# Performance work log

Hardware: AMD Instinct MI355X
Metric: run time of the kernel (lower is better)

The kernel has to match this reference:

```python
import jax, jax.numpy as jnp
import numpy as np

H = 1024


def _trilinear(q, k, w1, w2, w3):
    # q: [B, Lq, H], k: [B, Lk, H], w*: [H]
    ql = q @ w1                                  # [B, Lq]
    kl = k @ w2                                  # [B, Lk]
    dot = jnp.einsum('bqd,bkd->bqk', q, k * w3)  # [B, Lq, Lk]
    return ql[:, :, None] + kl[:, None, :] + dot


def _attention(q, k, v, qm, km, w1, w2, w3):
    # qm: [B, Lq] bool, km: [B, Lk] bool
    logit = _trilinear(q, k, w1, w2, w3)
    mask = qm[:, :, None] & km[:, None, :]
    logit = jnp.where(mask, logit, -jnp.inf)
    aw = jnp.where(mask, jax.nn.softmax(logit, axis=-1), 0.0)   # row softmax
    attn = aw @ v
    kq = jnp.where(mask, jax.nn.softmax(logit, axis=1), 0.0)    # column softmax
    co_w = aw @ jnp.swapaxes(kq, -1, -2)                        # [B, Lq, Lq]
    co_attn = co_w @ q
    return attn, co_attn


def setup_inputs() -> dict:
    key = jax.random.key(0)
    ks = jax.random.split(key, 20)
    B, S = 32, 1024
    def lin(k, out_d, in_d):
        kw, kb = jax.random.split(k)
        return (jax.random.normal(kw, (out_d, in_d), jnp.float32) * 0.02,
                jnp.zeros((out_d,), jnp.float32))
    comp_w, comp_b = lin(ks[3], H, 7 * H)
    gate_w, gate_b = lin(ks[4], H, 2 * H)
    attn_w, attn_b = lin(ks[5], H, 3 * H)
    self_w, self_b = lin(ks[6], H, 4 * H)
    tri = lambda k: jax.random.normal(k, (H,), jnp.float32) * 0.02
    return {
        'input_ids': jax.random.randint(ks[0], (B, S), 0, 30000, jnp.int32),
        'attention_mask': jnp.ones((B, S), jnp.int32),
        'doc_final_pos': 769,
        'num_label': 4,
        'last_layer': jax.random.normal(ks[1], (B, S, H), jnp.float32),
        'ow1': tri(ks[7]), 'ow2': tri(ks[8]), 'ow3': tri(ks[9]),
        'dw1': tri(ks[10]), 'dw2': tri(ks[11]), 'dw3': tri(ks[12]),
        'sw1': tri(ks[13]), 'sw2': tri(ks[14]), 'sw3': tri(ks[15]),
        'comp_w': comp_w, 'comp_b': comp_b,
        'gate_w': gate_w, 'gate_b': gate_b,
        'attn_w': attn_w, 'attn_b': attn_b,
        'self_w': self_w, 'self_b': self_b,
    }


def reference(input_ids, attention_mask, doc_final_pos, num_label, last_layer,
              ow1, ow2, ow3, dw1, dw2, dw3, sw1, sw2, sw3,
              comp_w, comp_b, gate_w, gate_b, attn_w, attn_b, self_w, self_b):
    bsz = input_ids.shape[0] // num_label
    p = doc_final_pos
    h = last_layer.shape[-1]
    doc_enc = last_layer[:, : p - 1, :]            # [B, Ld, H]
    opt_enc = last_layer[:, p - 1 :, :]            # [B, Lo, H]
    Lo = opt_enc.shape[1]
    doc_mask = attention_mask[:, : p - 1] > 0
    opt_mask4 = (attention_mask[:, p - 1 :] > 0).reshape(bsz, num_label, Lo)
    opt_enc4 = opt_enc.reshape(bsz, num_label, Lo, h)
    # pairwise option comparison
    corr = []
    for i in range(num_label):
        cur, cm = opt_enc4[:, i], opt_mask4[:, i]
        comp = [cur]
        for j in range(num_label):
            if j == i:
                continue
            a, _ = _attention(cur, opt_enc4[:, j], opt_enc4[:, j], cm, opt_mask4[:, j], ow1, ow2, ow3)
            comp.append(cur * a)
            comp.append(cur - a)
        corr.append(jnp.tanh(jnp.concatenate(comp, -1) @ comp_w.T + comp_b))
    opt_corr = jnp.stack(corr, axis=1).reshape(bsz * num_label, Lo, h)
    om = opt_mask4.reshape(bsz * num_label, Lo)
    gate = jax.nn.sigmoid(jnp.concatenate([opt_enc, opt_corr], -1) @ gate_w.T + gate_b)
    option = opt_enc * gate + opt_corr * (1.0 - gate)
    a, co = _attention(option, doc_enc, doc_enc, om, doc_mask, dw1, dw2, dw3)
    fusion = jax.nn.relu(jnp.concatenate([option, a, co], -1) @ attn_w.T + attn_b)
    sa, _ = _attention(fusion, fusion, fusion, om, om, sw1, sw2, sw3)
    fusion = jax.nn.relu(jnp.concatenate([fusion, sa, fusion * sa, fusion - sa], -1) @ self_w.T + self_b)
    fusion = jnp.where(om[:, :, None], fusion, -jnp.inf)
    return fusion.max(axis=1)  # [bsz*num_label, H]
```

## Files before the change

kernel.cpp:

```cpp
#include <hip/hip_runtime.h>

#define HDIM 1024
#define LLBS 1048576L
#define OPTBS 262144L
#define LDSP 72

typedef _Float16 f16;
typedef __attribute__((ext_vector_type(8))) _Float16 f16x8;
typedef __attribute__((ext_vector_type(4))) _Float16 f16x4;
typedef __attribute__((ext_vector_type(4))) float    f32x4;

__global__ __launch_bounds__(256)
void cvt_kernel(const float* __restrict__ src, f16* __restrict__ dst, long n)
{
  long i = ((long)blockIdx.x * 256 + threadIdx.x) * 8;
  const long stride = (long)gridDim.x * 256 * 8;
  for (; i < n; i += stride) {
    const float4 a = *(const float4*)(src + i);
    const float4 b = *(const float4*)(src + i + 4);
    *(f16x8*)(dst + i) = f16x8{(f16)a.x,(f16)a.y,(f16)a.z,(f16)a.w,
                               (f16)b.x,(f16)b.y,(f16)b.z,(f16)b.w};
  }
}

__device__ __forceinline__
void stage_rows(f16* __restrict__ sh, const f16* __restrict__ src, long rs, int t)
{
  const int row = t >> 1, h = (t & 1) << 5;
  const f16x8* p = (const f16x8*)(src + (long)row * rs + h);
  const f16x8 a = p[0], b = p[1], c = p[2], d = p[3];
  f16x8* q = (f16x8*)&sh[row * LDSP + h];
  q[0] = a; q[1] = b; q[2] = c; q[3] = d;
}

__device__ __forceinline__ f16x8 sc8(f16x8 v, const float* s)
{
  const float4 s0 = *(const float4*)s, s1 = *(const float4*)(s + 4);
  f16x8 r;
  r[0]=(f16)((float)v[0]*s0.x); r[1]=(f16)((float)v[1]*s0.y);
  r[2]=(f16)((float)v[2]*s0.z); r[3]=(f16)((float)v[3]*s0.w);
  r[4]=(f16)((float)v[4]*s1.x); r[5]=(f16)((float)v[5]*s1.y);
  r[6]=(f16)((float)v[6]*s1.z); r[7]=(f16)((float)v[7]*s1.w);
  return r;
}

__device__ __forceinline__
void stage_rows_scale(f16* __restrict__ sh, const f16* __restrict__ src, long rs,
                      const float* __restrict__ sc, int t)
{
  const int row = t >> 1, h = (t & 1) << 5;
  const f16x8* p = (const f16x8*)(src + (long)row * rs + h);
  f16x8* q = (f16x8*)&sh[row * LDSP + h];
  #pragma unroll
  for (int e = 0; e < 4; ++e) q[e] = sc8(p[e], sc + h + e * 8);
}

__device__ __forceinline__
void stage_vt(f16* __restrict__ sh, const f16* __restrict__ src, long rs, int t)
{
  const int jc = (t & 31) << 2, kg = (t >> 5) << 3;
  const f16* p = src + (long)kg * rs + jc;
  f16x4 r[8];
  #pragma unroll
  for (int e = 0; e < 8; ++e) r[e] = *(const f16x4*)(p + (long)e * rs);
  #pragma unroll
  for (int c = 0; c < 4; ++c) {
    *(f16x8*)&sh[(jc + c) * LDSP + kg] =
      f16x8{r[0][c], r[1][c], r[2][c], r[3][c], r[4][c], r[5][c], r[6][c], r[7][c]};
  }
}

__device__ __forceinline__
void mfma_step(const f16* __restrict__ Ash, const f16* __restrict__ Bsh, int t, f32x4 acc[4][4])
{
  const int lane = t & 63, wid = t >> 6;
  const int wm = (wid >> 1) << 6, wn = (wid & 1) << 6;
  const int r = lane & 15;
  #pragma unroll
  for (int kh = 0; kh < 2; ++kh) {
    const int kg = (kh << 5) + ((lane >> 4) << 3);
    f16x8 af[4], bf[4];
    #pragma unroll
    for (int m = 0; m < 4; ++m) af[m] = *(const f16x8*)&Ash[(wm + m * 16 + r) * LDSP + kg];
    #pragma unroll
    for (int n = 0; n < 4; ++n) bf[n] = *(const f16x8*)&Bsh[(wn + n * 16 + r) * LDSP + kg];
    #pragma unroll
    for (int m = 0; m < 4; ++m)
      #pragma unroll
      for (int n = 0; n < 4; ++n)
        acc[m][n] = __builtin_amdgcn_mfma_f32_16x16x32_f16(af[m], bf[n], acc[m][n], 0, 0, 0);
  }
}

template<int SCALE>
__device__ __forceinline__
void mm_at_core(f16* Ash, f16* Bsh, const f16* Ab, long Ars,
                const f16* Bb, long Brs, int K, const float* scale, int t, f32x4 acc[4][4])
{
  for (int k0 = 0; k0 < K; k0 += 64) {
    __syncthreads();
    stage_rows(Ash, Ab + k0, Ars, t);
    if (SCALE) stage_rows_scale(Bsh, Bb + k0, Brs, scale + k0, t);
    else       stage_rows(Bsh, Bb + k0, Brs, t);
    __syncthreads();
    mfma_step(Ash, Bsh, t, acc);
  }
}

__device__ __forceinline__
void mm_ab_core(f16* Ash, f16* Bsh, const f16* Ab, long Ars,
                const f16* Bb, long Brs, int K, int t, f32x4 acc[4][4])
{
  for (int k0 = 0; k0 < K; k0 += 64) {
    __syncthreads();
    stage_rows(Ash, Ab + k0, Ars, t);
    stage_vt(Bsh, Bb + (long)k0 * Brs, Brs, t);
    __syncthreads();
    mfma_step(Ash, Bsh, t, acc);
  }
}

template<int SCALE, int RANK1, int HOUT>
__global__ __launch_bounds__(256)
void mm_at_kernel(const f16* __restrict__ A, long Abs, long Ars,
                  const f16* __restrict__ B, long Bbs, long Brs, int K,
                  const float* __restrict__ scale,
                  const float* __restrict__ ql, long qlbs,
                  const float* __restrict__ kl, long klbs,
                  void* __restrict__ C, long Cbs, long Crs)
{
  __shared__ __align__(16) f16 Ash[128 * LDSP];
  __shared__ __align__(16) f16 Bsh[128 * LDSP];
  const int z = blockIdx.z, t = threadIdx.x;
  const int i0 = blockIdx.y << 7, j0 = blockIdx.x << 7;
  f32x4 acc[4][4] = {};
  mm_at_core<SCALE>(Ash, Bsh, A + (long)z * Abs + (long)i0 * Ars, Ars,
                    B + (long)z * Bbs + (long)j0 * Brs, Brs, K, scale, t, acc);
  const int lane = t & 63, wid = t >> 6;
  const int wm = (wid >> 1) << 6, wn = (wid & 1) << 6;
  const int rq = (lane >> 4) << 2, cj = lane & 15;
  #pragma unroll
  for (int m = 0; m < 4; ++m)
    #pragma unroll
    for (int q = 0; q < 4; ++q) {
      const int row = i0 + wm + m * 16 + rq + q;
      const float qv = RANK1 ? ql[(long)z * qlbs + row] : 0.f;
      #pragma unroll
      for (int n = 0; n < 4; ++n) {
        const int col = j0 + wn + n * 16 + cj;
        float v = acc[m][n][q] + qv;
        if (RANK1) v += kl[(long)z * klbs + col];
        if (HOUT) ((f16*)C)[(long)z * Cbs + (long)row * Crs + col] = (f16)v;
        else      ((float*)C)[(long)z * Cbs + (long)row * Crs + col] = v;
      }
    }
}

__global__ __launch_bounds__(256)
void mm_ab_kernel(const f16* __restrict__ A, long Abs, long Ars,
                  const f16* __restrict__ B, long Bbs, long Brs, int K,
                  f16* __restrict__ C, long Cbs, long Crs)
{
  __shared__ __align__(16) f16 Ash[128 * LDSP];
  __shared__ __align__(16) f16 Bsh[128 * LDSP];
  const int z = blockIdx.z, t = threadIdx.x;
  const int i0 = blockIdx.y << 7, j0 = blockIdx.x << 7;
  f32x4 acc[4][4] = {};
  mm_ab_core(Ash, Bsh, A + (long)z * Abs + (long)i0 * Ars, Ars,
             B + (long)z * Bbs + j0, Brs, K, t, acc);
  const int lane = t & 63, wid = t >> 6;
  const int wm = (wid >> 1) << 6, wn = (wid & 1) << 6;
  const int rq = (lane >> 4) << 2, cj = lane & 15;
  f16* Cb = C + (long)z * Cbs;
  #pragma unroll
  for (int m = 0; m < 4; ++m)
    #pragma unroll
    for (int q = 0; q < 4; ++q) {
      const int row = i0 + wm + m * 16 + rq + q;
      #pragma unroll
      for (int n = 0; n < 4; ++n) {
        const int col = j0 + wn + n * 16 + cj;
        Cb[(long)row * Crs + col] = (f16)acc[m][n][q];
      }
    }
}

__device__ __forceinline__ void pair_decode(int pair, int& i, int& j) {
  i = pair / 3; const int r = pair - i * 3; j = r + (r >= i ? 1 : 0);
}

__global__ __launch_bounds__(256)
void stA_logits_kernel(const f16* __restrict__ OPT, const float* __restrict__ w3,
                       const float* __restrict__ ql_all, const float* __restrict__ kl_all,
                       float* __restrict__ L)
{
  __shared__ __align__(16) f16 Ash[128 * LDSP];
  __shared__ __align__(16) f16 Bsh[128 * LDSP];
  const int z = blockIdx.z, t = threadIdx.x;
  const int pair = z >> 3, b8 = z & 7;
  int i, j; pair_decode(pair, i, j);
  const int bi = b8 * 4 + i, bj = b8 * 4 + j;
  const int i0 = blockIdx.y << 7, j0 = blockIdx.x << 7;
  f32x4 acc[4][4] = {};
  mm_at_core<1>(Ash, Bsh, OPT + (long)bi * LLBS + (long)i0 * HDIM, HDIM,
                OPT + (long)bj * LLBS + (long)j0 * HDIM, HDIM, HDIM, w3, t, acc);
  const float* qlp = ql_all + bi * 256;
  const float* klp = kl_all + bj * 256;
  float* Cb = L + (long)z * 65536;
  const int lane = t & 63, wid = t >> 6;
  const int wm = (wid >> 1) << 6, wn = (wid & 1) << 6;
  const int rq = (lane >> 4) << 2, cj = lane & 15;
  #pragma unroll
  for (int m = 0; m < 4; ++m)
    #pragma unroll
    for (int q = 0; q < 4; ++q) {
      const int row = i0 + wm + m * 16 + rq + q;
      const float qv = qlp[row];
      #pragma unroll
      for (int n = 0; n < 4; ++n) {
        const int col = j0 + wn + n * 16 + cj;
        Cb[(long)row * 256 + col] = acc[m][n][q] + qv + klp[col];
      }
    }
}

__global__ __launch_bounds__(256)
void stA_attn_kernel(const f16* __restrict__ P, const f16* __restrict__ OPT,
                     f16* __restrict__ aBuf)
{
  __shared__ __align__(16) f16 Ash[128 * LDSP];
  __shared__ __align__(16) f16 Bsh[128 * LDSP];
  const int z = blockIdx.z, t = threadIdx.x;
  const int pair = z >> 3, b8 = z & 7;
  int i, j; pair_decode(pair, i, j);
  const int bj = b8 * 4 + j;
  const int i0 = blockIdx.y << 7, j0 = blockIdx.x << 7;
  f32x4 acc[4][4] = {};
  mm_ab_core(Ash, Bsh, P + (long)z * 65536 + (long)i0 * 256, 256,
             OPT + (long)bj * LLBS + j0, HDIM, 256, t, acc);
  const int lane = t & 63, wid = t >> 6;
  const int wm = (wid >> 1) << 6, wn = (wid & 1) << 6;
  const int rq = (lane >> 4) << 2, cj = lane & 15;
  f16* Cb = aBuf + (long)z * OPTBS;
  #pragma unroll
  for (int m = 0; m < 4; ++m)
    #pragma unroll
    for (int q = 0; q < 4; ++q) {
      const int row = i0 + wm + m * 16 + rq + q;
      #pragma unroll
      for (int n = 0; n < 4; ++n)
        Cb[(long)row * HDIM + j0 + wn + n * 16 + cj] = (f16)acc[m][n][q];
    }
}

__global__ __launch_bounds__(256)
void stA_comp_kernel(const f16* __restrict__ OPT, const f16* __restrict__ aBuf,
                     const f16* __restrict__ W, const float* __restrict__ bias,
                     f16* __restrict__ out)
{
  __shared__ __align__(16) f16 Ash[128 * LDSP];
  __shared__ __align__(16) f16 Wsh[128 * LDSP];
  const int Lb = blockIdx.x, t = threadIdx.x;
  const int c = Lb & 7, w = Lb >> 3;
  const int n0 = (w >> 3) << 7;
  const int g = (c << 3) | (w & 7);
  const int i0 = (g & 1) << 7;
  const int z = g >> 1;
  const int b8 = z >> 2, i = z & 3;
  const f16* cur = OPT + (long)z * LLBS;
  const f16* a0 = aBuf + (long)((i * 3 + 0) * 8 + b8) * OPTBS;
  const f16* a1 = aBuf + (long)((i * 3 + 1) * 8 + b8) * OPTBS;
  const f16* a2 = aBuf + (long)((i * 3 + 2) * 8 + b8) * OPTBS;
  const f16* Wb = W + (long)n0 * 7168;
  f32x4 acc[4][4] = {};
  const int row = t >> 1, h = (t & 1) << 5;
  for (int k0 = 0; k0 < 7168; k0 += 64) {
    const int blk = k0 >> 10, kk = k0 & 1023;
    __syncthreads();
    {
      const long ro = (long)(i0 + row) * HDIM + kk + h;
      const f16x8* pc = (const f16x8*)(cur + ro);
      f16x8 a = pc[0], b = pc[1], cc = pc[2], d = pc[3];
      if (blk) {
        const int m = (blk - 1) >> 1;
        const f16* ap = (m == 0) ? a0 : (m == 1 ? a1 : a2);
        const f16x8* pa = (const f16x8*)(ap + ro);
        const f16x8 e = pa[0], f = pa[1], gg = pa[2], hh = pa[3];
        if (blk & 1) { a *= e; b *= f; cc *= gg; d *= hh; }
        else         { a -= e; b -= f; cc -= gg; d -= hh; }
      }
      f16x8* q = (f16x8*)&Ash[row * LDSP + h];
      q[0] = a; q[1] = b; q[2] = cc; q[3] = d;
    }
    stage_rows(Wsh, Wb + k0, 7168, t);
    __syncthreads();
    mfma_step(Ash, Wsh, t, acc);
  }
  const int lane = t & 63, wid = t >> 6;
  const int wm = (wid >> 1) << 6, wn = (wid & 1) << 6;
  const int rq = (lane >> 4) << 2, cj = lane & 15;
  f16* ob = out + (long)z * OPTBS;
  #pragma unroll
  for (int m = 0; m < 4; ++m)
    #pragma unroll
    for (int q = 0; q < 4; ++q) {
      const int r2 = i0 + wm + m * 16 + rq + q;
      #pragma unroll
      for (int n = 0; n < 4; ++n) {
        const int col = n0 + wn + n * 16 + cj;
        ob[(long)r2 * HDIM + col] = (f16)tanhf(acc[m][n][q] + bias[col]);
      }
    }
}

struct FCSrc { const f16* s0; const f16* s1; long s0bs; long s1bs; int op; int pad; };
struct FCArgs {
  FCSrc src[4];
  int nblk; int act;
  const f16* W; const float* bias;
  f16* out; long outbs;
  const f16* e0; const f16* e1; long e0bs; long e1bs;
};

__global__ __launch_bounds__(256)
void fc_mfma_kernel(FCArgs P)
{
  __shared__ __align__(16) f16 Ash[128 * LDSP];
  __shared__ __align__(16) f16 Wsh[128 * LDSP];
  const int Lb = blockIdx.x, t = threadIdx.x;
  const int c = Lb & 7, w = Lb >> 3;
  const int n0 = (w >> 3) << 7;
  const int g = (c << 3) | (w & 7);
  const int i0 = (g & 1) << 7;
  const int b = g >> 1;
  const int Ktot = P.nblk << 10;
  const f16* Wb = P.W + (long)n0 * Ktot;
  f32x4 acc[4][4] = {};
  const int row = t >> 1, h = (t & 1) << 5;
  for (int k0 = 0; k0 < Ktot; k0 += 64) {
    const FCSrc s = P.src[k0 >> 10];
    const int kk = k0 & 1023;
    __syncthreads();
    {
      const long ro = (long)(i0 + row) * HDIM + kk + h;
      const f16x8* p0 = (const f16x8*)(s.s0 + (long)b * s.s0bs + ro);
      f16x8 a = p0[0], bb = p0[1], cc = p0[2], d = p0[3];
      if (s.op) {
        const f16x8* p1 = (const f16x8*)(s.s1 + (long)b * s.s1bs + ro);
        const f16x8 e = p1[0], f = p1[1], gg = p1[2], hh = p1[3];
        if (s.op == 1) { a *= e; bb *= f; cc *= gg; d *= hh; }
        else           { a -= e; bb -= f; cc -= gg; d -= hh; }
      }
      f16x8* q = (f16x8*)&Ash[row * LDSP + h];
      q[0] = a; q[1] = bb; q[2] = cc; q[3] = d;
    }
    stage_rows(Wsh, Wb + k0, Ktot, t);
    __syncthreads();
    mfma_step(Ash, Wsh, t, acc);
  }
  const int lane = t & 63, wid = t >> 6;
  const int wm = (wid >> 1) << 6, wn = (wid & 1) << 6;
  const int rq = (lane >> 4) << 2, cj = lane & 15;
  #pragma unroll
  for (int m = 0; m < 4; ++m)
    #pragma unroll
    for (int q = 0; q < 4; ++q) {
      const int r2 = i0 + wm + m * 16 + rq + q;
      f16* orow = P.out + (long)b * P.outbs + (long)r2 * HDIM;
      #pragma unroll
      for (int n = 0; n < 4; ++n) {
        const int col = n0 + wn + n * 16 + cj;
        float v = acc[m][n][q] + P.bias[col];
        if (P.act == 0) v = tanhf(v);
        else if (P.act == 1) v = fmaxf(v, 0.f);
        else {
          const float sg = 1.f / (1.f + __expf(-v));
          const float e = (float)P.e0[(long)b * P.e0bs + (long)r2 * HDIM + col];
          const float c2 = (float)P.e1[(long)b * P.e1bs + (long)r2 * HDIM + col];
          v = e * sg + c2 * (1.f - sg);
        }
        orow[col] = (f16)v;
      }
    }
}

__global__ __launch_bounds__(256)
void rowdot_kernel(const f16* __restrict__ base, long bs, int R,
                   const float* __restrict__ w, float* __restrict__ out)
{
  const int row  = blockIdx.x * 4 + (threadIdx.x >> 6);
  const int lane = threadIdx.x & 63;
  const int b = row / R, r = row - b * R;
  const f16* p = base + (long)b * bs + (long)r * HDIM;
  float s = 0.f;
  #pragma unroll 4
  for (int d = lane; d < HDIM; d += 64) s += (float)p[d] * w[d];
  #pragma unroll
  for (int off = 32; off; off >>= 1) s += __shfl_down(s, off, 64);
  if (lane == 0) out[row] = s;
}

template<int CNT>
__global__ __launch_bounds__(256)
void softmax_rows_kernel(const float* __restrict__ L, f16* __restrict__ P)
{
  const int row = blockIdx.x * 4 + (threadIdx.x >> 6);
  const int lane = threadIdx.x & 63;
  const float* p = L + (long)row * (CNT * 64);
  f16* o = P + (long)row * (CNT * 64);
  float v[CNT];
  float m = -3.0e38f;
  #pragma unroll
  for (int u = 0; u < CNT; ++u) { v[u] = p[lane + (u << 6)]; m = fmaxf(m, v[u]); }
  #pragma unroll
  for (int off = 32; off; off >>= 1) m = fmaxf(m, __shfl_xor(m, off, 64));
  float s = 0.f;
  #pragma unroll
  for (int u = 0; u < CNT; ++u) { v[u] = __expf(v[u] - m); s += v[u]; }
  #pragma unroll
  for (int off = 32; off; off >>= 1) s += __shfl_xor(s, off, 64);
  const float inv = 1.f / s;
  #pragma unroll
  for (int u = 0; u < CNT; ++u) o[lane + (u << 6)] = (f16)(v[u] * inv);
}

__global__ __launch_bounds__(256)
void softmax_cols_kernel(const float* __restrict__ L, f16* __restrict__ out, int M, int N)
{
  const int b = blockIdx.y;
  const int j = blockIdx.x * 256 + threadIdx.x;
  const float* p = L + (long)b * M * N + j;
  f16* o = out + (long)b * M * N + j;
  float m = -3.0e38f;
  for (int i = 0; i < M; ++i) m = fmaxf(m, p[(long)i * N]);
  float s = 0.f;
  for (int i = 0; i < M; ++i) { const float e = __expf(p[(long)i * N] - m); o[(long)i * N] = (f16)e; s += e; }
  const float inv = 1.f / s;
  for (int i = 0; i < M; ++i) o[(long)i * N] = (f16)((float)o[(long)i * N] * inv);
}

__global__ __launch_bounds__(256)
void colmax_kernel(const f16* __restrict__ X, float* __restrict__ out)
{
  const int b = blockIdx.y;
  const int d = blockIdx.x * 256 + threadIdx.x;
  const f16* p = X + (long)b * (256 * HDIM) + d;
  float m = -3.0e38f;
  for (int r = 0; r < 256; ++r) m = fmaxf(m, (float)p[r * HDIM]);
  out[b * HDIM + d] = m;
}

extern "C" void kernel_launch(void* const* d_in, const int* in_sizes, int n_in,
                              void* d_out, int out_size, void* d_ws, size_t ws_size,
                              hipStream_t stream)
{
  (void)in_sizes; (void)n_in; (void)out_size; (void)ws_size;
  const float* last   = (const float*)d_in[4];
  const float* ow1    = (const float*)d_in[5];
  const float* ow2    = (const float*)d_in[6];
  const float* ow3    = (const float*)d_in[7];
  const float* dw1    = (const float*)d_in[8];
  const float* dw2    = (const float*)d_in[9];
  const float* dw3    = (const float*)d_in[10];
  const float* sw1    = (const float*)d_in[11];
  const float* sw2    = (const float*)d_in[12];
  const float* sw3    = (const float*)d_in[13];
  const float* comp_w = (const float*)d_in[14];
  const float* comp_b = (const float*)d_in[15];
  const float* gate_w = (const float*)d_in[16];
  const float* gate_b = (const float*)d_in[17];
  const float* attn_w = (const float*)d_in[18];
  const float* attn_b = (const float*)d_in[19];
  const float* self_w = (const float*)d_in[20];
  const float* self_b = (const float*)d_in[21];

  char* base = (char*)d_ws;
  size_t off = 0;
  auto af = [&](long n) { float* p = (float*)(base + off); off = (off + n * 4 + 15) & ~15UL; return p; };
  auto ah = [&](long n) { f16* p = (f16*)(base + off); off = (off + n * 2 + 15) & ~15UL; return p; };

  f16* lastH = ah(33554432L);
  f16* compH = ah(7340032L);
  f16* gateH = ah(2097152L);
  f16* attnH = ah(3145728L);
  f16* selfH = ah(4194304L);
  f16* aBuf  = ah(96L * OPTBS);
  f16* pA    = ah(96L * 65536);
  f16* awC   = ah(32L * 196608);
  f16* kqC   = ah(32L * 196608);
  f16* pE    = ah(32L * 65536);
  f16* co_wH = ah(32L * 65536);
  f16* buf1  = ah(32L * OPTBS);
  f16* buf2  = ah(32L * OPTBS);
  f16* buf3  = ah(32L * OPTBS);
  f16* buf4  = ah(32L * OPTBS);
  float* L   = af(32L * 196608);
  float* ql_all = af(8192); float* kl_all = af(8192);
  float* ql_c   = af(8192); float* kl_c   = af(24576);
  float* ql_e   = af(8192); float* kl_e   = af(8192);

  const f16* OPTH = lastH + 768 * 1024;

  cvt_kernel<<<2048, 256, 0, stream>>>(last,   lastH, 33554432L);
  cvt_kernel<<<512,  256, 0, stream>>>(comp_w, compH, 7340032L);
  cvt_kernel<<<256,  256, 0, stream>>>(gate_w, gateH, 2097152L);
  cvt_kernel<<<256,  256, 0, stream>>>(attn_w, attnH, 3145728L);
  cvt_kernel<<<256,  256, 0, stream>>>(self_w, selfH, 4194304L);

  rowdot_kernel<<<2048, 256, 0, stream>>>(OPTH, LLBS, 256, ow1, ql_all);
  rowdot_kernel<<<2048, 256, 0, stream>>>(OPTH, LLBS, 256, ow2, kl_all);
  stA_logits_kernel<<<dim3(2, 2, 96), 256, 0, stream>>>(OPTH, ow3, ql_all, kl_all, L);
  softmax_rows_kernel<4><<<(96 * 256) / 4, 256, 0, stream>>>(L, pA);
  stA_attn_kernel<<<dim3(8, 2, 96), 256, 0, stream>>>(pA, OPTH, aBuf);
  stA_comp_kernel<<<512, 256, 0, stream>>>(OPTH, aBuf, compH, comp_b, buf1);

  {
    FCArgs P = {};
    P.src[0] = {OPTH, nullptr, LLBS,  0, 0, 0};
    P.src[1] = {buf1, nullptr, OPTBS, 0, 0, 0};
    P.nblk = 2; P.act = 2; P.W = gateH; P.bias = gate_b;
    P.e0 = OPTH; P.e0bs = LLBS; P.e1 = buf1; P.e1bs = OPTBS;
    P.out = buf2; P.outbs = OPTBS;
    fc_mfma_kernel<<<512, 256, 0, stream>>>(P);
  }

  rowdot_kernel<<<2048, 256, 0, stream>>>(buf2, OPTBS, 256, dw1, ql_c);
  rowdot_kernel<<<6144, 256, 0, stream>>>(lastH, LLBS, 768, dw2, kl_c);
  mm_at_kernel<1, 1, 0><<<dim3(6, 2, 32), 256, 0, stream>>>(buf2, OPTBS, HDIM, lastH, LLBS, HDIM, HDIM,
                                                            dw3, ql_c, 256, kl_c, 768, L, 196608, 768);
  softmax_cols_kernel<<<dim3(3, 32), 256, 0, stream>>>(L, kqC, 256, 768);
  softmax_rows_kernel<12><<<8192 / 4, 256, 0, stream>>>(L, awC);
  mm_ab_kernel<<<dim3(8, 2, 32), 256, 0, stream>>>(awC, 196608, 768, lastH, LLBS, HDIM, 768,
                                                   buf1, OPTBS, HDIM);
  mm_at_kernel<0, 0, 1><<<dim3(2, 2, 32), 256, 0, stream>>>(awC, 196608, 768, kqC, 196608, 768, 768,
                                                            nullptr, nullptr, 0, nullptr, 0, co_wH, 65536, 256);
  mm_ab_kernel<<<dim3(8, 2, 32), 256, 0, stream>>>(co_wH, 65536, 256, buf2, OPTBS, HDIM, 256,
                                                   buf3, OPTBS, HDIM);

  {
    FCArgs P = {};
    P.src[0] = {buf2, nullptr, OPTBS, 0, 0, 0};
    P.src[1] = {buf1, nullptr, OPTBS, 0, 0, 0};
    P.src[2] = {buf3, nullptr, OPTBS, 0, 0, 0};
    P.nblk = 3; P.act = 1; P.W = attnH; P.bias = attn_b;
    P.out = buf4; P.outbs = OPTBS;
    fc_mfma_kernel<<<512, 256, 0, stream>>>(P);
  }

  rowdot_kernel<<<2048, 256, 0, stream>>>(buf4, OPTBS, 256, sw1, ql_e);
  rowdot_kernel<<<2048, 256, 0, stream>>>(buf4, OPTBS, 256, sw2, kl_e);
  mm_at_kernel<1, 1, 0><<<dim3(2, 2, 32), 256, 0, stream>>>(buf4, OPTBS, HDIM, buf4, OPTBS, HDIM, HDIM,
                                                            sw3, ql_e, 256, kl_e, 256, L, 65536, 256);
  softmax_rows_kernel<4><<<8192 / 4, 256, 0, stream>>>(L, pE);
  mm_ab_kernel<<<dim3(8, 2, 32), 256, 0, stream>>>(pE, 65536, 256, buf4, OPTBS, HDIM, 256,
                                                   buf2, OPTBS, HDIM);

  {
    FCArgs P = {};
    P.src[0] = {buf4, nullptr, OPTBS, 0, 0, 0};
    P.src[1] = {buf2, nullptr, OPTBS, 0, 0, 0};
    P.src[2] = {buf4, buf2, OPTBS, OPTBS, 1, 0};
    P.src[3] = {buf4, buf2, OPTBS, OPTBS, 2, 0};
    P.nblk = 4; P.act = 1; P.W = selfH; P.bias = self_b;
    P.out = buf3; P.outbs = OPTBS;
    fc_mfma_kernel<<<512, 256, 0, stream>>>(P);
  }

  colmax_kernel<<<dim3(4, 32), 256, 0, stream>>>(buf3, (float*)d_out);
}
```

Measured before the change: 1.348 ms.

## Double-buffer GEMM LDS tiles with async global-to-LDS loads and XOR swizzle

Every MFMA GEMM kernel now uses two LDS buffers per operand. The next K-slice is fetched while the current one feeds the MFMAs, leaving one barrier per iteration instead of two. Plain operand tiles are loaded straight into LDS with global_load_lds, and the padded layout is replaced by an XOR-swizzled 128-byte row layout to avoid bank conflicts. LDS use doubles to 64KB per block, which may reduce occupancy.

```diff
diff --git a/kernel.cpp b/kernel.cpp
--- a/kernel.cpp
+++ b/kernel.cpp
@@ -3,70 +3,82 @@
 #define HDIM 1024
 #define LLBS 1048576L
 #define OPTBS 262144L
-#define LDSP 72
 
 typedef _Float16 f16;
 typedef __attribute__((ext_vector_type(8))) _Float16 f16x8;
 typedef __attribute__((ext_vector_type(4))) _Float16 f16x4;
 typedef __attribute__((ext_vector_type(4))) float    f32x4;
 
-__global__ __launch_bounds__(256)
-void cvt_kernel(const float* __restrict__ src, f16* __restrict__ dst, long n)
-{
-  long i = ((long)blockIdx.x * 256 + threadIdx.x) * 8;
-  const long stride = (long)gridDim.x * 256 * 8;
-  for (; i < n; i += stride) {
-    const float4 a = *(const float4*)(src + i);
-    const float4 b = *(const float4*)(src + i + 4);
-    *(f16x8*)(dst + i) = f16x8{(f16)a.x,(f16)a.y,(f16)a.z,(f16)a.w,
-                               (f16)b.x,(f16)b.y,(f16)b.z,(f16)b.w};
-  }
+__device__ __forceinline__ char* swzp(f16* tile, int row, int colb) {
+  return (char*)tile + (row << 7) + (colb ^ ((row & 7) << 4));
+}
+__device__ __forceinline__ const char* swzp(const f16* tile, int row, int colb) {
+  return (const char*)tile + (row << 7) + (colb ^ ((row & 7) << 4));
+}
+
+__device__ __forceinline__ void gload16(const f16* g, f16* l) {
+  __builtin_amdgcn_global_load_lds((const __attribute__((address_space(1))) void*)g,
+                                   (__attribute__((address_space(3))) void*)l, 16, 0, 0);
 }
 
 __device__ __forceinline__
-void stage_rows(f16* __restrict__ sh, const f16* __restrict__ src, long rs, int t)
-{
-  const int row = t >> 1, h = (t & 1) << 5;
-  const f16x8* p = (const f16x8*)(src + (long)row * rs + h);
-  const f16x8 a = p[0], b = p[1], c = p[2], d = p[3];
-  f16x8* q = (f16x8*)&sh[row * LDSP + h];
-  q[0] = a; q[1] = b; q[2] = c; q[3] = d;
-}
-
-__device__ __forceinline__ f16x8 sc8(f16x8 v, const float* s)
-{
-  const float4 s0 = *(const float4*)s, s1 = *(const float4*)(s + 4);
-  f16x8 r;
-  r[0]=(f16)((float)v[0]*s0.x); r[1]=(f16)((float)v[1]*s0.y);
-  r[2]=(f16)((float)v[2]*s0.z); r[3]=(f16)((float)v[3]*s0.w);
-  r[4]=(f16)((float)v[4]*s1.x); r[5]=(f16)((float)v[5]*s1.y);
-  r[6]=(f16)((float)v[6]*s1.z); r[7]=(f16)((float)v[7]*s1.w);
-  return r;
-}
-
-__device__ __forceinline__
-void stage_rows_scale(f16* __restrict__ sh, const f16* __restrict__ src, long rs,
-                      const float* __restrict__ sc, int t)
-{
-  const int row = t >> 1, h = (t & 1) << 5;
-  const f16x8* p = (const f16x8*)(src + (long)row * rs + h);
-  f16x8* q = (f16x8*)&sh[row * LDSP + h];
-  #pragma unroll
-  for (int e = 0; e < 4; ++e) q[e] = sc8(p[e], sc + h + e * 8);
-}
-
-__device__ __forceinline__
-void stage_vt(f16* __restrict__ sh, const f16* __restrict__ src, long rs, int t)
-{
+void stage_g(f16* __restrict__ tile, const f16* __restrict__ src, long rs, int t)
+{
+  const int l = t & 63, w = t >> 6;
+  const int rsub = l >> 3;
+  const int csub = ((l & 7) ^ rsub) << 3;
+  const f16* gp = src + (long)rsub * rs + csub;
+  #pragma unroll
+  for (int p = 0; p < 4; ++p) {
+    const int i = (w << 2) + p;
+    gload16(gp + (long)(i << 3) * rs, tile + (i << 9));
+  }
+}
+
+struct VT { f16x4 r[8]; };
+__device__ __forceinline__ VT vt_load(const f16* __restrict__ src, long rs, int t) {
   const int jc = (t & 31) << 2, kg = (t >> 5) << 3;
   const f16* p = src + (long)kg * rs + jc;
-  f16x4 r[8];
-  #pragma unroll
-  for (int e = 0; e < 8; ++e) r[e] = *(const f16x4*)(p + (long)e * rs);
-  #pragma unroll
-  for (int c = 0; c < 4; ++c) {
-    *(f16x8*)&sh[(jc + c) * LDSP + kg] =
-      f16x8{r[0][c], r[1][c], r[2][c], r[3][c], r[4][c], r[5][c], r[6][c], r[7][c]};
+  VT v;
+  #pragma unroll
+  for (int e = 0; e < 8; ++e) v.r[e] = *(const f16x4*)(p + (long)e * rs);
+  return v;
+}
+__device__ __forceinline__ void vt_write(f16* __restrict__ tile, const VT& v, int t) {
+  const int jc = (t & 31) << 2, kg = (t >> 5) << 3;
+  #pragma unroll
+  for (int c = 0; c < 4; ++c)
+    *(f16x8*)swzp(tile, jc + c, kg << 1) =
+      f16x8{v.r[0][c], v.r[1][c], v.r[2][c], v.r[3][c],
+            v.r[4][c], v.r[5][c], v.r[6][c], v.r[7][c]};
+}
+
+__device__ __forceinline__ void ld4(f16x8 v[4], const f16* p) {
+  const f16x8* q = (const f16x8*)p;
+  v[0] = q[0]; v[1] = q[1]; v[2] = q[2]; v[3] = q[3];
+}
+__device__ __forceinline__ void a_write(f16* __restrict__ tile, const f16x8 v[4], int t) {
+  const int row = t >> 1, h2 = (t & 1) << 6;
+  #pragma unroll
+  for (int e = 0; e < 4; ++e)
+    *(f16x8*)swzp(tile, row, h2 + (e << 4)) = v[e];
+}
+__device__ __forceinline__
+void sc_load(f16x8 v[4], const f16* __restrict__ src, long rs,
+             const float* __restrict__ sc, int t)
+{
+  const int row = t >> 1, h = (t & 1) << 5;
+  ld4(v, src + (long)row * rs + h);
+  #pragma unroll
+  for (int e = 0; e < 4; ++e) {
+    const float4 s0 = *(const float4*)(sc + h + e * 8);
+    const float4 s1 = *(const float4*)(sc + h + e * 8 + 4);
+    f16x8 x = v[e];
+    x[0]=(f16)((float)x[0]*s0.x); x[1]=(f16)((float)x[1]*s0.y);
+    x[2]=(f16)((float)x[2]*s0.z); x[3]=(f16)((float)x[3]*s0.w);
+    x[4]=(f16)((float)x[4]*s1.x); x[5]=(f16)((float)x[5]*s1.y);
+    x[6]=(f16)((float)x[6]*s1.z); x[7]=(f16)((float)x[7]*s1.w);
+    v[e] = x;
   }
 }
 
@@ -78,12 +90,12 @@
   const int r = lane & 15;
   #pragma unroll
   for (int kh = 0; kh < 2; ++kh) {
-    const int kg = (kh << 5) + ((lane >> 4) << 3);
+    const int kb = ((kh << 5) | ((lane >> 4) << 3)) << 1;
     f16x8 af[4], bf[4];
     #pragma unroll
-    for (int m = 0; m < 4; ++m) af[m] = *(const f16x8*)&Ash[(wm + m * 16 + r) * LDSP + kg];
-    #pragma unroll
-    for (int n = 0; n < 4; ++n) bf[n] = *(const f16x8*)&Bsh[(wn + n * 16 + r) * LDSP + kg];
+    for (int m = 0; m < 4; ++m) af[m] = *(const f16x8*)swzp(Ash, wm + m * 16 + r, kb);
+    #pragma unroll
+    for (int n = 0; n < 4; ++n) bf[n] = *(const f16x8*)swzp(Bsh, wn + n * 16 + r, kb);
     #pragma unroll
     for (int m = 0; m < 4; ++m)
       #pragma unroll
@@ -92,50 +104,60 @@
   }
 }
 
-template<int SCALE>
+template<int BMODE>
 __device__ __forceinline__
-void mm_at_core(f16* Ash, f16* Bsh, const f16* Ab, long Ars,
-                const f16* Bb, long Brs, int K, const float* scale, int t, f32x4 acc[4][4])
-{
-  for (int k0 = 0; k0 < K; k0 += 64) {
+void mm_body(f16* A0, f16* A1, f16* B0, f16* B1,
+             const f16* __restrict__ Ab, long Ars,
+             const f16* __restrict__ Bb, long Brs, int K,
+             const float* __restrict__ scale, int t, f32x4 acc[4][4])
+{
+  stage_g(A0, Ab, Ars, t);
+  if (BMODE == 1) { VT v = vt_load(Bb, Brs, t); vt_write(B0, v, t); }
+  else if (BMODE == 2) { f16x8 v[4]; sc_load(v, Bb, Brs, scale, t); a_write(B0, v, t); }
+  else stage_g(B0, Bb, Brs, t);
+  __syncthreads();
+  f16 *Ac = A0, *An = A1, *Bc = B0, *Bn = B1;
+  for (int k0 = 64; k0 < K; k0 += 64) {
+    stage_g(An, Ab + k0, Ars, t);
+    if (BMODE == 1) {
+      VT v = vt_load(Bb + (long)k0 * Brs, Brs, t);
+      mfma_step(Ac, Bc, t, acc);
+      vt_write(Bn, v, t);
+    } else if (BMODE == 2) {
+      f16x8 v[4]; sc_load(v, Bb + k0, Brs, scale + k0, t);
+      mfma_step(Ac, Bc, t, acc);
+      a_write(Bn, v, t);
+    } else {
+      stage_g(Bn, Bb + k0, Brs, t);
+      mfma_step(Ac, Bc, t, acc);
+    }
     __syncthreads();
-    stage_rows(Ash, Ab + k0, Ars, t);
-    if (SCALE) stage_rows_scale(Bsh, Bb + k0, Brs, scale + k0, t);
-    else       stage_rows(Bsh, Bb + k0, Brs, t);
-    __syncthreads();
-    mfma_step(Ash, Bsh, t, acc);
-  }
-}
-
-__device__ __forceinline__
-void mm_ab_core(f16* Ash, f16* Bsh, const f16* Ab, long Ars,
-                const f16* Bb, long Brs, int K, int t, f32x4 acc[4][4])
-{
-  for (int k0 = 0; k0 < K; k0 += 64) {
-    __syncthreads();
-    stage_rows(Ash, Ab + k0, Ars, t);
-    stage_vt(Bsh, Bb + (long)k0 * Brs, Brs, t);
-    __syncthreads();
-    mfma_step(Ash, Bsh, t, acc);
-  }
-}
-
-template<int SCALE, int RANK1, int HOUT>
-__global__ __launch_bounds__(256)
-void mm_at_kernel(const f16* __restrict__ A, long Abs, long Ars,
-                  const f16* __restrict__ B, long Bbs, long Brs, int K,
-                  const float* __restrict__ scale,
-                  const float* __restrict__ ql, long qlbs,
-                  const float* __restrict__ kl, long klbs,
-                  void* __restrict__ C, long Cbs, long Crs)
-{
-  __shared__ __align__(16) f16 Ash[128 * LDSP];
-  __shared__ __align__(16) f16 Bsh[128 * LDSP];
+    f16* x = Ac; Ac = An; An = x; x = Bc; Bc = Bn; Bn = x;
+  }
+  mfma_step(Ac, Bc, t, acc);
+}
+
+#define DECL_TILES \
+  __shared__ __align__(16) f16 A0[8192]; __shared__ __align__(16) f16 A1[8192]; \
+  __shared__ __align__(16) f16 B0[8192]; __shared__ __align__(16) f16 B1[8192];
+
+template<int BMODE, int RANK1, int HOUT>
+__global__ __launch_bounds__(256)
+void mm_kernel(const f16* __restrict__ A, long Abs, long Ars,
+               const f16* __restrict__ B, long Bbs, long Brs, int K,
+               const float* __restrict__ scale,
+               const float* __restrict__ ql, long qlbs,
+               const float* __restrict__ kl, long klbs,
+               void* __restrict__ C, long Cbs, long Crs)
+{
+  DECL_TILES
   const int z = blockIdx.z, t = threadIdx.x;
   const int i0 = blockIdx.y << 7, j0 = blockIdx.x << 7;
+  const f16* Ab = A + (long)z * Abs + (long)i0 * Ars;
+  const f16* Bb = (BMODE == 1) ? (B + (long)z * Bbs + j0)
+                               : (B + (long)z * Bbs + (long)j0 * Brs);
   f32x4 acc[4][4] = {};
-  mm_at_core<SCALE>(Ash, Bsh, A + (long)z * Abs + (long)i0 * Ars, Ars,
-                    B + (long)z * Bbs + (long)j0 * Brs, Brs, K, scale, t, acc);
+  mm_body<BMODE>(A0, A1, B0, B1, Ab, Ars, Bb, Brs, K, scale, t, acc);
   const int lane = t & 63, wid = t >> 6;
   const int wm = (wid >> 1) << 6, wn = (wid & 1) << 6;
   const int rq = (lane >> 4) << 2, cj = lane & 15;
@@ -156,35 +178,6 @@
     }
 }
 
-__global__ __launch_bounds__(256)
-void mm_ab_kernel(const f16* __restrict__ A, long Abs, long Ars,
-                  const f16* __restrict__ B, long Bbs, long Brs, int K,
-                  f16* __restrict__ C, long Cbs, long Crs)
-{
-  __shared__ __align__(16) f16 Ash[128 * LDSP];
-  __shared__ __align__(16) f16 Bsh[128 * LDSP];
-  const int z = blockIdx.z, t = threadIdx.x;
-  const int i0 = blockIdx.y << 7, j0 = blockIdx.x << 7;
-  f32x4 acc[4][4] = {};
-  mm_ab_core(Ash, Bsh, A + (long)z * Abs + (long)i0 * Ars, Ars,
-             B + (long)z * Bbs + j0, Brs, K, t, acc);
-  const int lane = t & 63, wid = t >> 6;
-  const int wm = (wid >> 1) << 6, wn = (wid & 1) << 6;
-  const int rq = (lane >> 4) << 2, cj = lane & 15;
-  f16* Cb = C + (long)z * Cbs;
-  #pragma unroll
-  for (int m = 0; m < 4; ++m)
-    #pragma unroll
-    for (int q = 0; q < 4; ++q) {
-      const int row = i0 + wm + m * 16 + rq + q;
-      #pragma unroll
-      for (int n = 0; n < 4; ++n) {
-        const int col = j0 + wn + n * 16 + cj;
-        Cb[(long)row * Crs + col] = (f16)acc[m][n][q];
-      }
-    }
-}
-
 __device__ __forceinline__ void pair_decode(int pair, int& i, int& j) {
   i = pair / 3; const int r = pair - i * 3; j = r + (r >= i ? 1 : 0);
 }
@@ -194,16 +187,15 @@
                        const float* __restrict__ ql_all, const float* __restrict__ kl_all,
                        float* __restrict__ L)
 {
-  __shared__ __align__(16) f16 Ash[128 * LDSP];
-  __shared__ __align__(16) f16 Bsh[128 * LDSP];
+  DECL_TILES
   const int z = blockIdx.z, t = threadIdx.x;
   const int pair = z >> 3, b8 = z & 7;
   int i, j; pair_decode(pair, i, j);
   const int bi = b8 * 4 + i, bj = b8 * 4 + j;
   const int i0 = blockIdx.y << 7, j0 = blockIdx.x << 7;
   f32x4 acc[4][4] = {};
-  mm_at_core<1>(Ash, Bsh, OPT + (long)bi * LLBS + (long)i0 * HDIM, HDIM,
-                OPT + (long)bj * LLBS + (long)j0 * HDIM, HDIM, HDIM, w3, t, acc);
+  mm_body<2>(A0, A1, B0, B1, OPT + (long)bi * LLBS + (long)i0 * HDIM, HDIM,
+             OPT + (long)bj * LLBS + (long)j0 * HDIM, HDIM, HDIM, w3, t, acc);
   const float* qlp = ql_all + bi * 256;
   const float* klp = kl_all + bj * 256;
   float* Cb = L + (long)z * 65536;
@@ -228,16 +220,15 @@
 void stA_attn_kernel(const f16* __restrict__ P, const f16* __restrict__ OPT,
                      f16* __restrict__ aBuf)
 {
-  __shared__ __align__(16) f16 Ash[128 * LDSP];
-  __shared__ __align__(16) f16 Bsh[128 * LDSP];
+  DECL_TILES
   const int z = blockIdx.z, t = threadIdx.x;
   const int pair = z >> 3, b8 = z & 7;
   int i, j; pair_decode(pair, i, j);
   const int bj = b8 * 4 + j;
   const int i0 = blockIdx.y << 7, j0 = blockIdx.x << 7;
   f32x4 acc[4][4] = {};
-  mm_ab_core(Ash, Bsh, P + (long)z * 65536 + (long)i0 * 256, 256,
-             OPT + (long)bj * LLBS + j0, HDIM, 256, t, acc);
+  mm_body<1>(A0, A1, B0, B1, P + (long)z * 65536 + (long)i0 * 256, 256,
+             OPT + (long)bj * LLBS + j0, HDIM, 256, nullptr, t, acc);
   const int lane = t & 63, wid = t >> 6;
   const int wm = (wid >> 1) << 6, wn = (wid & 1) << 6;
   const int rq = (lane >> 4) << 2, cj = lane & 15;
@@ -258,8 +249,7 @@
                      const f16* __restrict__ W, const float* __restrict__ bias,
                      f16* __restrict__ out)
 {
-  __shared__ __align__(16) f16 Ash[128 * LDSP];
-  __shared__ __align__(16) f16 Wsh[128 * LDSP];
+  DECL_TILES
   const int Lb = blockIdx.x, t = threadIdx.x;
   const int c = Lb & 7, w = Lb >> 3;
   const int n0 = (w >> 3) << 7;
@@ -272,30 +262,41 @@
   const f16* a1 = aBuf + (long)((i * 3 + 1) * 8 + b8) * OPTBS;
   const f16* a2 = aBuf + (long)((i * 3 + 2) * 8 + b8) * OPTBS;
   const f16* Wb = W + (long)n0 * 7168;
+  const int row = t >> 1, h = (t & 1) << 5;
+  const long rbase = (long)(i0 + row) * HDIM + h;
   f32x4 acc[4][4] = {};
-  const int row = t >> 1, h = (t & 1) << 5;
-  for (int k0 = 0; k0 < 7168; k0 += 64) {
+  f16x8 r0[4], r1[4];
+  auto aload = [&](int k0) {
     const int blk = k0 >> 10, kk = k0 & 1023;
+    const long ro = rbase + kk;
+    ld4(r0, cur + ro);
+    if (blk) {
+      const int m = (blk - 1) >> 1;
+      const f16* ap = (m == 0) ? a0 : (m == 1 ? a1 : a2);
+      ld4(r1, ap + ro);
+    }
+  };
+  auto aop = [&](int k0) {
+    const int blk = k0 >> 10;
+    if (blk) {
+      if (blk & 1) { r0[0]*=r1[0]; r0[1]*=r1[1]; r0[2]*=r1[2]; r0[3]*=r1[3]; }
+      else         { r0[0]-=r1[0]; r0[1]-=r1[1]; r0[2]-=r1[2]; r0[3]-=r1[3]; }
+    }
+  };
+  aload(0); aop(0); a_write(A0, r0, t);
+  stage_g(B0, Wb, 7168, t);
+  __syncthreads();
+  f16 *Ac = A0, *An = A1, *Wc = B0, *Wn = B1;
+  for (int k0 = 64; k0 < 7168; k0 += 64) {
+    aload(k0);
+    stage_g(Wn, Wb + k0, 7168, t);
+    mfma_step(Ac, Wc, t, acc);
+    aop(k0);
+    a_write(An, r0, t);
     __syncthreads();
-    {
-      const long ro = (long)(i0 + row) * HDIM + kk + h;
-      const f16x8* pc = (const f16x8*)(cur + ro);
-      f16x8 a = pc[0], b = pc[1], cc = pc[2], d = pc[3];
-      if (blk) {
-        const int m = (blk - 1) >> 1;
-        const f16* ap = (m == 0) ? a0 : (m == 1 ? a1 : a2);
-        const f16x8* pa = (const f16x8*)(ap + ro);
-        const f16x8 e = pa[0], f = pa[1], gg = pa[2], hh = pa[3];
-        if (blk & 1) { a *= e; b *= f; cc *= gg; d *= hh; }
-        else         { a -= e; b -= f; cc -= gg; d -= hh; }
-      }
-      f16x8* q = (f16x8*)&Ash[row * LDSP + h];
-      q[0] = a; q[1] = b; q[2] = cc; q[3] = d;
-    }
-    stage_rows(Wsh, Wb + k0, 7168, t);
-    __syncthreads();
-    mfma_step(Ash, Wsh, t, acc);
-  }
+    f16* x = Ac; Ac = An; An = x; x = Wc; Wc = Wn; Wn = x;
+  }
+  mfma_step(Ac, Wc, t, acc);
   const int lane = t & 63, wid = t >> 6;
   const int wm = (wid >> 1) << 6, wn = (wid & 1) << 6;
   const int rq = (lane >> 4) << 2, cj = lane & 15;
@@ -325,8 +326,7 @@
 __global__ __launch_bounds__(256)
 void fc_mfma_kernel(FCArgs P)
 {
-  __shared__ __align__(16) f16 Ash[128 * LDSP];
-  __shared__ __align__(16) f16 Wsh[128 * LDSP];
+  DECL_TILES
   const int Lb = blockIdx.x, t = threadIdx.x;
   const int c = Lb & 7, w = Lb >> 3;
   const int n0 = (w >> 3) << 7;
@@ -335,29 +335,37 @@
   const int b = g >> 1;
   const int Ktot = P.nblk << 10;
   const f16* Wb = P.W + (long)n0 * Ktot;
+  const int row = t >> 1, h = (t & 1) << 5;
+  const long rbase = (long)(i0 + row) * HDIM + h;
   f32x4 acc[4][4] = {};
-  const int row = t >> 1, h = (t & 1) << 5;
-  for (int k0 = 0; k0 < Ktot; k0 += 64) {
+  f16x8 r0[4], r1[4];
+  int opc = 0;
+  auto aload = [&](int k0) {
     const FCSrc s = P.src[k0 >> 10];
     const int kk = k0 & 1023;
+    const long ro = rbase + kk;
+    opc = s.op;
+    ld4(r0, s.s0 + (long)b * s.s0bs + ro);
+    if (opc) ld4(r1, s.s1 + (long)b * s.s1bs + ro);
+  };
+  auto aop = [&]() {
+    if (opc == 1)      { r0[0]*=r1[0]; r0[1]*=r1[1]; r0[2]*=r1[2]; r0[3]*=r1[3]; }
+    else if (opc == 2) { r0[0]-=r1[0]; r0[1]-=r1[1]; r0[2]-=r1[2]; r0[3]-=r1[3]; }
+  };
+  aload(0); aop(); a_write(A0, r0, t);
+  stage_g(B0, Wb, Ktot, t);
+  __syncthreads();
+  f16 *Ac = A0, *An = A1, *Wc = B0, *Wn = B1;
+  for (int k0 = 64; k0 < Ktot; k0 += 64) {
+    aload(k0);
+    stage_g(Wn, Wb + k0, Ktot, t);
+    mfma_step(Ac, Wc, t, acc);
+    aop();
+    a_write(An, r0, t);
     __syncthreads();
-    {
-      const long ro = (long)(i0 + row) * HDIM + kk + h;
-      const f16x8* p0 = (const f16x8*)(s.s0 + (long)b * s.s0bs + ro);
-      f16x8 a = p0[0], bb = p0[1], cc = p0[2], d = p0[3];
-      if (s.op) {
-        const f16x8* p1 = (const f16x8*)(s.s1 + (long)b * s.s1bs + ro);
-        const f16x8 e = p1[0], f = p1[1], gg = p1[2], hh = p1[3];
-        if (s.op == 1) { a *= e; bb *= f; cc *= gg; d *= hh; }
-        else           { a -= e; bb -= f; cc -= gg; d -= hh; }
-      }
-      f16x8* q = (f16x8*)&Ash[row * LDSP + h];
-      q[0] = a; q[1] = bb; q[2] = cc; q[3] = d;
-    }
-    stage_rows(Wsh, Wb + k0, Ktot, t);
-    __syncthreads();
-    mfma_step(Ash, Wsh, t, acc);
-  }
+    f16* x = Ac; Ac = An; An = x; x = Wc; Wc = Wn; Wn = x;
+  }
+  mfma_step(Ac, Wc, t, acc);
   const int lane = t & 63, wid = t >> 6;
   const int wm = (wid >> 1) << 6, wn = (wid & 1) << 6;
   const int rq = (lane >> 4) << 2, cj = lane & 15;
@@ -382,6 +390,19 @@
         orow[col] = (f16)v;
       }
     }
+}
+
+__global__ __launch_bounds__(256)
+void cvt_kernel(const float* __restrict__ src, f16* __restrict__ dst, long n)
+{
+  long i = ((long)blockIdx.x * 256 + threadIdx.x) * 8;
+  const long stride = (long)gridDim.x * 2048;
+  for (; i < n; i += stride) {
+    const float4 a = *(const float4*)(src + i);
+    const float4 b = *(const float4*)(src + i + 4);
+    *(f16x8*)(dst + i) = f16x8{(f16)a.x,(f16)a.y,(f16)a.z,(f16)a.w,
+                               (f16)b.x,(f16)b.y,(f16)b.z,(f16)b.w};
+  }
 }
 
 __global__ __launch_bounds__(256)
@@ -526,16 +547,16 @@
 
   rowdot_kernel<<<2048, 256, 0, stream>>>(buf2, OPTBS, 256, dw1, ql_c);
   rowdot_kernel<<<6144, 256, 0, stream>>>(lastH, LLBS, 768, dw2, kl_c);
-  mm_at_kernel<1, 1, 0><<<dim3(6, 2, 32), 256, 0, stream>>>(buf2, OPTBS, HDIM, lastH, LLBS, HDIM, HDIM,
-                                                            dw3, ql_c, 256, kl_c, 768, L, 196608, 768);
+  mm_kernel<2, 1, 0><<<dim3(6, 2, 32), 256, 0, stream>>>(buf2, OPTBS, HDIM, lastH, LLBS, HDIM, HDIM,
+                                                         dw3, ql_c, 256, kl_c, 768, L, 196608, 768);
   softmax_cols_kernel<<<dim3(3, 32), 256, 0, stream>>>(L, kqC, 256, 768);
   softmax_rows_kernel<12><<<8192 / 4, 256, 0, stream>>>(L, awC);
-  mm_ab_kernel<<<dim3(8, 2, 32), 256, 0, stream>>>(awC, 196608, 768, lastH, LLBS, HDIM, 768,
-                                                   buf1, OPTBS, HDIM);
-  mm_at_kernel<0, 0, 1><<<dim3(2, 2, 32), 256, 0, stream>>>(awC, 196608, 768, kqC, 196608, 768, 768,
-                                                            nullptr, nullptr, 0, nullptr, 0, co_wH, 65536, 256);
-  mm_ab_kernel<<<dim3(8, 2, 32), 256, 0, stream>>>(co_wH, 65536, 256, buf2, OPTBS, HDIM, 256,
-                                                   buf3, OPTBS, HDIM);
+  mm_kernel<1, 0, 1><<<dim3(8, 2, 32), 256, 0, stream>>>(awC, 196608, 768, lastH, LLBS, HDIM, 768,
+                                                         nullptr, nullptr, 0, nullptr, 0, buf1, OPTBS, HDIM);
+  mm_kernel<0, 0, 1><<<dim3(2, 2, 32), 256, 0, stream>>>(awC, 196608, 768, kqC, 196608, 768, 768,
+                                                         nullptr, nullptr, 0, nullptr, 0, co_wH, 65536, 256);
+  mm_kernel<1, 0, 1><<<dim3(8, 2, 32), 256, 0, stream>>>(co_wH, 65536, 256, buf2, OPTBS, HDIM, 256,
+                                                         nullptr, nullptr, 0, nullptr, 0, buf3, OPTBS, HDIM);
 
   {
     FCArgs P = {};
@@ -549,11 +570,11 @@
 
   rowdot_kernel<<<2048, 256, 0, stream>>>(buf4, OPTBS, 256, sw1, ql_e);
   rowdot_kernel<<<2048, 256, 0, stream>>>(buf4, OPTBS, 256, sw2, kl_e);
-  mm_at_kernel<1, 1, 0><<<dim3(2, 2, 32), 256, 0, stream>>>(buf4, OPTBS, HDIM, buf4, OPTBS, HDIM, HDIM,
-                                                            sw3, ql_e, 256, kl_e, 256, L, 65536, 256);
+  mm_kernel<2, 1, 0><<<dim3(2, 2, 32), 256, 0, stream>>>(buf4, OPTBS, HDIM, buf4, OPTBS, HDIM, HDIM,
+                                                         sw3, ql_e, 256, kl_e, 256, L, 65536, 256);
   softmax_rows_kernel<4><<<8192 / 4, 256, 0, stream>>>(L, pE);
-  mm_ab_kernel<<<dim3(8, 2, 32), 256, 0, stream>>>(pE, 65536, 256, buf4, OPTBS, HDIM, 256,
-                                                   buf2, OPTBS, HDIM);
+  mm_kernel<1, 0, 1><<<dim3(8, 2, 32), 256, 0, stream>>>(pE, 65536, 256, buf4, OPTBS, HDIM, 256,
+                                                         nullptr, nullptr, 0, nullptr, 0, buf2, OPTBS, HDIM);
 
   {
     FCArgs P = {};
```

After: 1.761 ms. 30.6% more time.
